# Kernel optimization log

Hardware: AMD Instinct MI355X
Metric: run time of the kernel (lower is better)

## Reference

```python
import jax, jax.numpy as jnp
import numpy as np

ROPE_BASE = 10000.0
NUM_HEADS = 16
NUM_KV_HEADS = 4


def _rms_norm(x, eps):
    # F.rms_norm with no weight: x / sqrt(mean(x^2) + eps)
    return x * jax.lax.rsqrt(jnp.mean(x * x, axis=-1, keepdims=True) + eps)


def _apply_rope(x, cos, sin):
    h = x.shape[-1] // 2
    x1, x2 = x[..., :h], x[..., h:]
    return jnp.concatenate([x1 * cos + x2 * sin, -x1 * sin + x2 * cos], axis=-1)


def setup_inputs() -> dict:
    key = jax.random.key(0)
    ks = jax.random.split(key, 5)
    B, T, D = 2, 2048, 1024
    H, Hkv = NUM_HEADS, NUM_KV_HEADS
    hd = D // H
    kv_dim = Hkv * hd
    s_in = 1.0 / np.sqrt(D)
    return {
        "x": jax.random.normal(ks[0], (B, T, D), dtype=jnp.float32),
        "Wq": jax.random.normal(ks[1], (D, D), dtype=jnp.float32) * s_in,
        "Wk": jax.random.normal(ks[2], (kv_dim, D), dtype=jnp.float32) * s_in,
        "Wv": jax.random.normal(ks[3], (kv_dim, D), dtype=jnp.float32) * s_in,
        "Wproj": jax.random.normal(ks[4], (D, D), dtype=jnp.float32) * s_in,
        "q_gain": jnp.full((H,), 1.0, dtype=jnp.float32),
    }


def reference(x, Wq, Wk, Wv, Wproj, q_gain):
    B, T, D = x.shape
    H, Hkv = NUM_HEADS, NUM_KV_HEADS
    hd = D // H
    rep = H // Hkv
    eps = jnp.finfo(x.dtype).eps

    # QKV projections (F.linear: x @ W.T)
    q = jnp.einsum('btd,od->bto', x, Wq).reshape(B, T, H, hd).transpose(0, 2, 1, 3)
    k = jnp.einsum('btd,od->bto', x, Wk).reshape(B, T, Hkv, hd).transpose(0, 2, 1, 3)
    v = jnp.einsum('btd,od->bto', x, Wv).reshape(B, T, Hkv, hd).transpose(0, 2, 1, 3)

    q = _rms_norm(q, eps)
    k = _rms_norm(k, eps)

    # RoPE tables: [1, 1, T, hd/2]
    inv_freq = 1.0 / (ROPE_BASE ** (jnp.arange(0, hd, 2, dtype=jnp.float32) / hd))
    f = jnp.arange(T, dtype=jnp.float32)[:, None] * inv_freq[None, :]
    cos = jnp.cos(f)[None, None].astype(q.dtype)
    sin = jnp.sin(f)[None, None].astype(q.dtype)
    q = _apply_rope(q, cos, sin)
    k = _apply_rope(k, cos, sin)

    q = q * q_gain.astype(q.dtype)[None, :, None, None]

    # GQA without materializing repeated K/V: group q heads [Hkv, rep]
    qg = q.reshape(B, Hkv, rep, T, hd)
    scale = hd ** -0.5
    scores = jnp.einsum('bgrqd,bgkd->bgrqk', qg, k) * scale
    causal = jnp.tril(jnp.ones((T, T), dtype=bool))
    scores = jnp.where(causal, scores, -jnp.inf)
    att = jax.nn.softmax(scores.astype(jnp.float32), axis=-1).astype(q.dtype)
    y = jnp.einsum('bgrqk,bgkd->bgrqd', att, v)  # [B,Hkv,rep,T,hd]
    y = y.reshape(B, H, T, hd).transpose(0, 2, 1, 3).reshape(B, T, D)
    return jnp.einsum('btd,od->bto', y, Wproj)
```

## Files before the change

kernel.cpp:

```cpp
#include <hip/hip_runtime.h>
#include <cstdint>
#include <cstddef>

typedef __attribute__((ext_vector_type(8))) short short8;
typedef __attribute__((ext_vector_type(4))) float floatx4;
typedef __attribute__((ext_vector_type(16))) float floatx16;
typedef __attribute__((ext_vector_type(4))) short short4v;
typedef unsigned short u16;
typedef unsigned int u32;

#define B_   2
#define T_   2048
#define D_   1024
#define H_   16
#define HKV_ 4
#define HD_  64
#define KV_  256
#define M_   4096
#define QS_  1536

#define NX   4194304
#define NWQ  1048576
#define NWK  262144
#define NWV  262144
#define NWP  1048576
#define NCAST (NX + NWQ + NWK + NWV + NWP)
#define CAST_BLOCKS (NCAST / 1024)
#define TAB_BLOCKS  256

__device__ __forceinline__ float b2f(u16 u) {
    union { u32 i; float f; } v; v.i = ((u32)u) << 16; return v.f;
}
__device__ __forceinline__ u16 f2b(float f) {
    union { float f; u32 i; } v; v.f = f;
    u32 r = v.i + 0x7FFF + ((v.i >> 16) & 1);
    return (u16)(r >> 16);
}
__device__ __forceinline__ u32 pack_hi(float a, float b) {
    union { float f; u32 u; } ua, ub; ua.f = a; ub.f = b;
    return (ua.u >> 16) | (ub.u & 0xFFFF0000u);
}

__device__ __forceinline__ void async16(const u16* g, u16* l) {
    __builtin_amdgcn_global_load_lds(
        (const __attribute__((address_space(1))) u32*)g,
        (__attribute__((address_space(3))) u32*)l, 16, 0, 0);
}

__device__ __forceinline__ u32 cvtpk(float lo, float hi) {
    u32 r;
    asm("v_cvt_pk_bf16_f32 %0, %1, %2" : "=v"(r) : "v"(lo), "v"(hi));
    return r;
}
__device__ __forceinline__ void swap32(u32& a, u32& b) {
    asm volatile("v_permlane32_swap_b32 %0, %1" : "+v"(a), "+v"(b));
}
__device__ __forceinline__ void swap32f(float& a, float& b) {
    asm volatile("v_permlane32_swap_b32 %0, %1" : "+v"(a), "+v"(b));
}
__device__ __forceinline__ short8 pkfrag(u32 w0, u32 w1, u32 w2, u32 w3) {
    union { u32 w[4]; short8 s; } u;
    u.w[0] = w0; u.w[1] = w1; u.w[2] = w2; u.w[3] = w3;
    return u.s;
}

__global__ __launch_bounds__(256) void prep(const float* __restrict__ x,
                                            const float* __restrict__ wq,
                                            const float* __restrict__ wk,
                                            const float* __restrict__ wv,
                                            const float* __restrict__ wp,
                                            u16* __restrict__ dst,
                                            float2* __restrict__ tab) {
    int blk = blockIdx.x;
    if (blk < CAST_BLOCKS) {
        int i = blk * 1024 + threadIdx.x * 4;
        const float* src; int off;
        if      (i < NX)                  { src = x;  off = i; }
        else if (i < NX+NWQ)              { src = wq; off = i - NX; }
        else if (i < NX+NWQ+NWK)          { src = wk; off = i - (NX+NWQ); }
        else if (i < NX+NWQ+NWK+NWV)      { src = wv; off = i - (NX+NWQ+NWK); }
        else                              { src = wp; off = i - (NX+NWQ+NWK+NWV); }
        float4 v = *(const float4*)(src + off);
        short4v o;
        o.x = (short)f2b(v.x); o.y = (short)f2b(v.y);
        o.z = (short)f2b(v.z); o.w = (short)f2b(v.w);
        *(short4v*)(dst + i) = o;
    } else {
        int idx = (blk - CAST_BLOCKS) * 256 + threadIdx.x;
        int t = idx >> 5, i = idx & 31;
        float freq = exp2f(-(float)i * (13.287712379549449f / 32.0f));
        float ang = (float)t * freq;
        tab[idx] = make_float2(cosf(ang), sinf(ang));
    }
}

__global__ __launch_bounds__(256, 3) void gemm_qkv(const u16* __restrict__ A,
                                                   const u16* __restrict__ W,
                                                   u16* __restrict__ C,
                                                   u16* __restrict__ Vt,
                                                   const float* __restrict__ gain,
                                                   const float2* __restrict__ tab) {
    const int K = D_;
    __shared__ u16 As[2][2][128 * 32];
    __shared__ u16 Bs[2][2][64 * 32];
    const int t = threadIdx.x;
    const int wave = t >> 6, lane = t & 63;
    const int quad = lane >> 4, l16 = lane & 15;
    const int wm = wave * 32;
    const int m0 = blockIdx.y * 128, n0 = blockIdx.x * 64;

    floatx4 acc[2][4];
#pragma unroll
    for (int i = 0; i < 2; i++)
#pragma unroll
        for (int j = 0; j < 4; j++) acc[i][j] = (floatx4){0.f, 0.f, 0.f, 0.f};

    const int sr = t >> 2, sc = (t & 3) * 8;
    const u16* ga = A + (size_t)(m0 + sr) * K + sc;
    const u16* gb = W + (size_t)(n0 + sr) * K + sc;

    auto stage = [&](int buf, int half, int koff) {
        async16(ga + koff, As[buf][half] + t * 8);
        async16(ga + koff + (size_t)64 * K, As[buf][half] + t * 8 + 64 * 32);
        async16(gb + koff, Bs[buf][half] + t * 8);
    };

    stage(0, 0, 0);
    stage(0, 1, 32);

    int cur = 0;
    for (int kt = 0; kt < K; kt += 64) {
        __syncthreads();
        if (kt + 64 < K) {
            stage(cur ^ 1, 0, kt + 64);
            stage(cur ^ 1, 1, kt + 96);
        }
#pragma unroll
        for (int half = 0; half < 2; half++) {
            short8 af[2], bf[4];
#pragma unroll
            for (int mt = 0; mt < 2; mt++)
                af[mt] = *(const short8*)(As[cur][half] + (wm + mt * 16 + l16) * 32 + quad * 8);
#pragma unroll
            for (int nt = 0; nt < 4; nt++)
                bf[nt] = *(const short8*)(Bs[cur][half] + (nt * 16 + l16) * 32 + quad * 8);
#pragma unroll
            for (int mt = 0; mt < 2; mt++)
#pragma unroll
                for (int nt = 0; nt < 4; nt++)
                    acc[mt][nt] = __builtin_amdgcn_mfma_f32_16x16x32_bf16(
                        af[mt], bf[nt], acc[mt][nt], 0, 0, 0);
        }
        cur ^= 1;
    }

    const int col0 = n0;
    if (col0 < 1280) {
        float gs = (col0 < 1024)
                 ? gain[col0 >> 6] * (0.125f * 1.4426950408889634f)
                 : 1.0f;
#pragma unroll
        for (int mt = 0; mt < 2; mt++)
#pragma unroll
            for (int r = 0; r < 4; r++) {
                int row = m0 + wm + mt * 16 + quad * 4 + r;
                int tt = row & (T_ - 1);
                float v0 = acc[mt][0][r], v1 = acc[mt][1][r];
                float v2 = acc[mt][2][r], v3 = acc[mt][3][r];
                float ss = v0 * v0 + v1 * v1 + v2 * v2 + v3 * v3;
                ss += __shfl_xor(ss, 1); ss += __shfl_xor(ss, 2);
                ss += __shfl_xor(ss, 4); ss += __shfl_xor(ss, 8);
                float inv = rsqrtf(ss * (1.0f / 64.0f) + 1.1920929e-7f);
                v0 *= inv; v1 *= inv; v2 *= inv; v3 *= inv;
                float2 cs0 = tab[tt * 32 + l16];
                float2 cs1 = tab[tt * 32 + 16 + l16];
                float o0 = (v0 * cs0.x + v2 * cs0.y) * gs;
                float o1 = (v1 * cs1.x + v3 * cs1.y) * gs;
                float o2 = (v2 * cs0.x - v0 * cs0.y) * gs;
                float o3 = (v3 * cs1.x - v1 * cs1.y) * gs;
                u16* cp = C + (size_t)row * QS_ + col0 + l16;
                cp[0]  = f2b(o0);
                cp[16] = f2b(o1);
                cp[32] = f2b(o2);
                cp[48] = f2b(o3);
            }
    } else {
        const int g = (col0 - 1280) >> 6;
#pragma unroll
        for (int mt = 0; mt < 2; mt++)
#pragma unroll
            for (int r = 0; r < 4; r++) {
                int row = m0 + wm + mt * 16 + quad * 4 + r;
                int tt = row & (T_ - 1);
                int bb = row >> 11;
#pragma unroll
                for (int nt = 0; nt < 4; nt++)
                    Vt[(size_t)((bb * 4 + g) * 64 + nt * 16 + l16) * T_ + tt] =
                        f2b(acc[mt][nt][r]);
            }
    }
}

__global__ __launch_bounds__(256, 3) void gemm_proj(const u16* __restrict__ A,
                                                    const u16* __restrict__ W,
                                                    float* __restrict__ C) {
    const int K = D_;
    __shared__ u16 As[2][2][128 * 32];
    __shared__ u16 Bs[2][2][64 * 32];
    const int t = threadIdx.x;
    const int wave = t >> 6, lane = t & 63;
    const int quad = lane >> 4, l16 = lane & 15;
    const int wm = wave * 32;
    const int m0 = blockIdx.y * 128, n0 = blockIdx.x * 64;

    floatx4 acc[2][4];
#pragma unroll
    for (int i = 0; i < 2; i++)
#pragma unroll
        for (int j = 0; j < 4; j++) acc[i][j] = (floatx4){0.f, 0.f, 0.f, 0.f};

    const int sr = t >> 2, sc = (t & 3) * 8;
    const u16* ga = A + (size_t)(m0 + sr) * K + sc;
    const u16* gb = W + (size_t)(n0 + sr) * K + sc;

    auto stage = [&](int buf, int half, int koff) {
        async16(ga + koff, As[buf][half] + t * 8);
        async16(ga + koff + (size_t)64 * K, As[buf][half] + t * 8 + 64 * 32);
        async16(gb + koff, Bs[buf][half] + t * 8);
    };

    stage(0, 0, 0);
    stage(0, 1, 32);

    int cur = 0;
    for (int kt = 0; kt < K; kt += 64) {
        __syncthreads();
        if (kt + 64 < K) {
            stage(cur ^ 1, 0, kt + 64);
            stage(cur ^ 1, 1, kt + 96);
        }
#pragma unroll
        for (int half = 0; half < 2; half++) {
            short8 af[2], bf[4];
#pragma unroll
            for (int mt = 0; mt < 2; mt++)
                af[mt] = *(const short8*)(As[cur][half] + (wm + mt * 16 + l16) * 32 + quad * 8);
#pragma unroll
            for (int nt = 0; nt < 4; nt++)
                bf[nt] = *(const short8*)(Bs[cur][half] + (nt * 16 + l16) * 32 + quad * 8);
#pragma unroll
            for (int mt = 0; mt < 2; mt++)
#pragma unroll
                for (int nt = 0; nt < 4; nt++)
                    acc[mt][nt] = __builtin_amdgcn_mfma_f32_16x16x32_bf16(
                        af[mt], bf[nt], acc[mt][nt], 0, 0, 0);
        }
        cur ^= 1;
    }

#pragma unroll
    for (int mt = 0; mt < 2; mt++)
#pragma unroll
        for (int nt = 0; nt < 4; nt++)
#pragma unroll
            for (int r = 0; r < 4; r++) {
                int row = m0 + wm + mt * 16 + quad * 4 + r;
                int col = n0 + nt * 16 + l16;
                C[(size_t)row * D_ + col] = acc[mt][nt][r];
            }
}

__global__ __launch_bounds__(256, 2) void flash(const u16* __restrict__ QKV,
                                                const u16* __restrict__ Vtr,
                                                float* __restrict__ Opart,
                                                float* __restrict__ Lpart) {
    const int u  = blockIdx.x;
    const int h  = blockIdx.y;
    const int b  = blockIdx.z;
    const int g  = h >> 2;
    const int w    = threadIdx.x >> 6;
    const int lane = threadIdx.x & 63;
    const int ln31 = lane & 31;
    const int hi   = lane >> 5;
    const int swz  = lane & 7;

    __shared__ u16 Kb[3][4096];
    __shared__ u16 Vb[3][4096];
    __shared__ float Ot[4][2048];

    const int srow = w * 16 + (lane >> 3);
    const int sseg = (lane & 7) ^ ((lane >> 3) & 7);
    const u16* kgb = QKV + (size_t)(b * T_ + srow) * QS_ + D_ + g * 64 + sseg * 8;
    const u16* vgb = Vtr + (size_t)((b * 4 + g) * 64 + srow) * T_ + sseg * 8;

    auto stage = [&](int tile, int bi) {
        const u16* kg = kgb + (size_t)tile * 64 * QS_;
        const u16* vg = vgb + (size_t)tile * 64;
        u16* kl = &Kb[bi][w * 1024 + lane * 8];
        u16* vl = &Vb[bi][w * 1024 + lane * 8];
        async16(kg, kl);
        async16(kg + (size_t)8 * QS_, kl + 512);
        async16(vg, vl);
        async16(vg + (size_t)8 * T_, vl + 512);
    };
    auto tileOf = [&](int gidx) { return (gidx <= u) ? gidx : gidx + 15 - 2 * u; };

    stage(tileOf(0), 0);
    stage(tileOf(1), 1);

    int gi = 0;
    for (int seg = 0; seg < 2; ++seg) {
        const int jt   = seg ? 15 - u : u;
        const int nIt  = seg ? 16 - u : u + 1;
        const int qrow = jt * 128 + w * 32 + ln31;

        const u16* qp = QKV + (size_t)(b * T_ + qrow) * QS_ + h * HD_;
        short8 aq[4];
#pragma unroll
        for (int kc = 0; kc < 4; kc++)
            aq[kc] = *(const short8*)(qp + kc * 16 + hi * 8);

        floatx16 acc[2];
#pragma unroll
        for (int dh = 0; dh < 2; dh++)
#pragma unroll
            for (int i = 0; i < 16; i++) acc[dh][i] = 0.f;
        float l = 0.f;

        for (int itn = 0; itn < nIt; ++itn, ++gi) {
            const int tk = tileOf(gi);
            if (gi == 16) asm volatile("s_waitcnt vmcnt(0)" ::: "memory");
            else          asm volatile("s_waitcnt vmcnt(4)" ::: "memory");
            __builtin_amdgcn_s_barrier();
            asm volatile("" ::: "memory");

            const int bc = gi % 3;
            if (gi + 2 <= 16) stage(tileOf(gi + 2), (gi + 2) % 3);

            const u16* Kp = &Kb[bc][0];
            const u16* Vp = &Vb[bc][0];
            short8 kf[2][4], vfr[2][4];
#pragma unroll
            for (int kh = 0; kh < 2; kh++)
#pragma unroll
                for (int kc = 0; kc < 4; kc++)
                    kf[kh][kc] = *(const short8*)(Kp + (kh * 32 + ln31) * 64 +
                                                  (((kc * 2 + hi) ^ swz) << 3));
#pragma unroll
            for (int dh = 0; dh < 2; dh++)
#pragma unroll
                for (int kc = 0; kc < 4; kc++)
                    vfr[dh][kc] = *(const short8*)(Vp + (dh * 32 + ln31) * 64 +
                                                   (((kc * 2 + hi) ^ swz) << 3));

            floatx16 s[2];
#pragma unroll
            for (int kh = 0; kh < 2; kh++)
#pragma unroll
                for (int i = 0; i < 16; i++) s[kh][i] = 0.f;

            __builtin_amdgcn_s_setprio(1);
#pragma unroll
            for (int kc = 0; kc < 4; kc++) {
                s[0] = __builtin_amdgcn_mfma_f32_32x32x16_bf16(kf[0][kc], aq[kc], s[0], 0, 0, 0);
                s[1] = __builtin_amdgcn_mfma_f32_32x32x16_bf16(kf[1][kc], aq[kc], s[1], 0, 0, 0);
            }
            __builtin_amdgcn_s_setprio(0);

            float p[2][16];
            if (tk >= 2 * jt) {
#pragma unroll
                for (int kh = 0; kh < 2; kh++)
#pragma unroll
                    for (int r = 0; r < 16; r++) {
                        int key = tk * 64 + kh * 32 + (r & 3) + ((r >> 2) << 3) + (hi << 2);
                        float e = __builtin_amdgcn_exp2f(s[kh][r]);
                        e = (key <= qrow) ? e : 0.f;
                        l += e; p[kh][r] = e;
                    }
            } else {
#pragma unroll
                for (int kh = 0; kh < 2; kh++)
#pragma unroll
                    for (int r = 0; r < 16; r++) {
                        float e = __builtin_amdgcn_exp2f(s[kh][r]);
                        l += e; p[kh][r] = e;
                    }
            }

            short8 pb[4];
#pragma unroll
            for (int kh = 0; kh < 2; kh++) {
                u32 a0 = cvtpk(p[kh][0], p[kh][1]),  b0 = cvtpk(p[kh][4], p[kh][5]);
                u32 c0 = cvtpk(p[kh][2], p[kh][3]),  d0 = cvtpk(p[kh][6], p[kh][7]);
                swap32(a0, b0); swap32(c0, d0);
                pb[kh * 2] = pkfrag(a0, c0, b0, d0);
                u32 a1 = cvtpk(p[kh][8],  p[kh][9]),  b1 = cvtpk(p[kh][12], p[kh][13]);
                u32 c1 = cvtpk(p[kh][10], p[kh][11]), d1 = cvtpk(p[kh][14], p[kh][15]);
                swap32(a1, b1); swap32(c1, d1);
                pb[kh * 2 + 1] = pkfrag(a1, c1, b1, d1);
            }

            __builtin_amdgcn_s_setprio(1);
#pragma unroll
            for (int kc = 0; kc < 4; kc++) {
                acc[0] = __builtin_amdgcn_mfma_f32_32x32x16_bf16(vfr[0][kc], pb[kc], acc[0], 0, 0, 0);
                acc[1] = __builtin_amdgcn_mfma_f32_32x32x16_bf16(vfr[1][kc], pb[kc], acc[1], 0, 0, 0);
            }
            __builtin_amdgcn_s_setprio(0);
        }

        float la = l, lb = l;
        swap32f(la, lb);
        float lt = la + lb;

        float* ot = &Ot[w][0];
#pragma unroll
        for (int dh = 0; dh < 2; dh++)
#pragma unroll
            for (int g4 = 0; g4 < 4; g4++) {
                int ss = (dh * 8 + g4 * 2 + hi) ^ (ln31 & 7);
                float4 v = make_float4(acc[dh][g4 * 4 + 0], acc[dh][g4 * 4 + 1],
                                       acc[dh][g4 * 4 + 2], acc[dh][g4 * 4 + 3]);
                *(float4*)(ot + ln31 * 64 + ss * 4) = v;
            }
        asm volatile("s_waitcnt lgkmcnt(0)" ::: "memory");

        const int hq = lane >> 4;
        const int s4 = lane & 15;
        float* obase = Opart + (size_t)seg * 4194304 +
                       ((size_t)(b * 2048 + jt * 128 + w * 32)) * 1024 + h * HD_;
#pragma unroll
        for (int it = 0; it < 8; it++) {
            int q2 = it * 4 + hq;
            int ss = s4 ^ (q2 & 7);
            float4 v = *(const float4*)(ot + q2 * 64 + ss * 4);
            *(float4*)(obase + (size_t)q2 * 1024 + s4 * 4) = v;
        }
        if (lane < 32)
            Lpart[((size_t)seg * 4096 + b * 2048 + jt * 128 + w * 32 + lane) * 16 + h] = lt;
    }
}

__global__ __launch_bounds__(256) void combine(const float* __restrict__ Opart,
                                               const float* __restrict__ Lpart,
                                               u16* __restrict__ Y) {
    int e = (blockIdx.x * 256 + threadIdx.x) * 4;
    int row = e >> 10, col = e & 1023;
    int li = row * 16 + (col >> 6);
    float l0 = Lpart[li];
    float l1 = Lpart[li + 4096 * 16];
    float inv = 1.0f / (l0 + l1);
    size_t oi = (size_t)row * 1024 + col;
    float4 o0 = *(const float4*)(Opart + oi);
    float4 o1 = *(const float4*)(Opart + oi + (size_t)4194304);
    short4v y;
    y.x = (short)f2b((o0.x + o1.x) * inv); y.y = (short)f2b((o0.y + o1.y) * inv);
    y.z = (short)f2b((o0.z + o1.z) * inv); y.w = (short)f2b((o0.w + o1.w) * inv);
    *(short4v*)(Y + (size_t)row * D_ + col) = y;
}

extern "C" void kernel_launch(void* const* d_in, const int* in_sizes, int n_in,
                              void* d_out, int out_size, void* d_ws, size_t ws_size,
                              hipStream_t stream) {
    const float* x    = (const float*)d_in[0];
    const float* Wq   = (const float*)d_in[1];
    const float* Wk   = (const float*)d_in[2];
    const float* Wv   = (const float*)d_in[3];
    const float* Wp   = (const float*)d_in[4];
    const float* gain = (const float*)d_in[5];
    float* out = (float*)d_out;

    u16* xb   = (u16*)d_ws;
    u16* Wcat = xb + (size_t)NX;
    u16* Wpb  = Wcat + (size_t)(NWQ + NWK + NWV);
    u16* QKV  = Wpb + (size_t)NWP;
    u16* Vt   = QKV + (size_t)M_ * QS_;
    u16* Y    = Vt + (size_t)M_ * KV_;
    float2* tab = (float2*)(Y + (size_t)M_ * D_);
    float* Opart = (float*)(tab + 65536);
    float* Lpart = Opart + (size_t)8 * 1024 * 1024;

    prep<<<CAST_BLOCKS + TAB_BLOCKS, 256, 0, stream>>>(x, Wq, Wk, Wv, Wp, xb, tab);

    gemm_qkv<<<dim3(QS_ / 64, M_ / 128), 256, 0, stream>>>(xb, Wcat, QKV, Vt,
                                                           gain, tab);

    flash<<<dim3(16, H_, B_), 256, 0, stream>>>(QKV, Vt, Opart, Lpart);

    combine<<<4096, 256, 0, stream>>>(Opart, Lpart, Y);

    gemm_proj<<<dim3(D_ / 64, M_ / 128), 256, 0, stream>>>(Y, Wpb, out);
}
```

Before: 164.5 us.

## Rebalance flash causal tiles, write low tiles directly, swizzle GEMM LDS layout

The causal work split in flash changes. Blocks with u<8 fully process query tile u and write the normalized bf16 output straight to Y. They then take the first part of tile 15-u, while blocks with u>=8 cover the rest of their own tile. Only the upper half of query rows now go through the Opart/Lpart partial buffers, which halves the combine kernel's work and the fp32 partial traffic. It also applies an XOR swizzle to the GEMM LDS tiles to cut bank conflicts on fragment reads, and packs softmax probabilities into bf16 pairs as they are computed. The tile-index mapping is intricate and risks load imbalance or indexing errors.

```diff
diff --git a/kernel.cpp b/kernel.cpp
--- a/kernel.cpp
+++ b/kernel.cpp
@@ -35,10 +35,6 @@
     union { float f; u32 i; } v; v.f = f;
     u32 r = v.i + 0x7FFF + ((v.i >> 16) & 1);
     return (u16)(r >> 16);
-}
-__device__ __forceinline__ u32 pack_hi(float a, float b) {
-    union { float f; u32 u; } ua, ub; ua.f = a; ub.f = b;
-    return (ua.u >> 16) | (ub.u & 0xFFFF0000u);
 }
 
 __device__ __forceinline__ void async16(const u16* g, u16* l) {
@@ -115,7 +111,8 @@
 #pragma unroll
         for (int j = 0; j < 4; j++) acc[i][j] = (floatx4){0.f, 0.f, 0.f, 0.f};
 
-    const int sr = t >> 2, sc = (t & 3) * 8;
+    const int sr = t >> 2;
+    const int sc = (((t & 3) ^ ((t >> 3) & 3)) * 8);
     const u16* ga = A + (size_t)(m0 + sr) * K + sc;
     const u16* gb = W + (size_t)(n0 + sr) * K + sc;
 
@@ -139,11 +136,17 @@
         for (int half = 0; half < 2; half++) {
             short8 af[2], bf[4];
 #pragma unroll
-            for (int mt = 0; mt < 2; mt++)
-                af[mt] = *(const short8*)(As[cur][half] + (wm + mt * 16 + l16) * 32 + quad * 8);
-#pragma unroll
-            for (int nt = 0; nt < 4; nt++)
-                bf[nt] = *(const short8*)(Bs[cur][half] + (nt * 16 + l16) * 32 + quad * 8);
+            for (int mt = 0; mt < 2; mt++) {
+                int row = wm + mt * 16 + l16;
+                af[mt] = *(const short8*)(As[cur][half] + row * 32 +
+                                          ((quad ^ ((row >> 1) & 3)) << 3));
+            }
+#pragma unroll
+            for (int nt = 0; nt < 4; nt++) {
+                int row = nt * 16 + l16;
+                bf[nt] = *(const short8*)(Bs[cur][half] + row * 32 +
+                                          ((quad ^ ((row >> 1) & 3)) << 3));
+            }
 #pragma unroll
             for (int mt = 0; mt < 2; mt++)
 #pragma unroll
@@ -219,7 +222,8 @@
 #pragma unroll
         for (int j = 0; j < 4; j++) acc[i][j] = (floatx4){0.f, 0.f, 0.f, 0.f};
 
-    const int sr = t >> 2, sc = (t & 3) * 8;
+    const int sr = t >> 2;
+    const int sc = (((t & 3) ^ ((t >> 3) & 3)) * 8);
     const u16* ga = A + (size_t)(m0 + sr) * K + sc;
     const u16* gb = W + (size_t)(n0 + sr) * K + sc;
 
@@ -243,11 +247,17 @@
         for (int half = 0; half < 2; half++) {
             short8 af[2], bf[4];
 #pragma unroll
-            for (int mt = 0; mt < 2; mt++)
-                af[mt] = *(const short8*)(As[cur][half] + (wm + mt * 16 + l16) * 32 + quad * 8);
-#pragma unroll
-            for (int nt = 0; nt < 4; nt++)
-                bf[nt] = *(const short8*)(Bs[cur][half] + (nt * 16 + l16) * 32 + quad * 8);
+            for (int mt = 0; mt < 2; mt++) {
+                int row = wm + mt * 16 + l16;
+                af[mt] = *(const short8*)(As[cur][half] + row * 32 +
+                                          ((quad ^ ((row >> 1) & 3)) << 3));
+            }
+#pragma unroll
+            for (int nt = 0; nt < 4; nt++) {
+                int row = nt * 16 + l16;
+                bf[nt] = *(const short8*)(Bs[cur][half] + row * 32 +
+                                          ((quad ^ ((row >> 1) & 3)) << 3));
+            }
 #pragma unroll
             for (int mt = 0; mt < 2; mt++)
 #pragma unroll
@@ -272,6 +282,7 @@
 
 __global__ __launch_bounds__(256, 2) void flash(const u16* __restrict__ QKV,
                                                 const u16* __restrict__ Vtr,
+                                                u16* __restrict__ Y,
                                                 float* __restrict__ Opart,
                                                 float* __restrict__ Lpart) {
     const int u  = blockIdx.x;
@@ -303,15 +314,21 @@
         async16(vg, vl);
         async16(vg + (size_t)8 * T_, vl + 512);
     };
-    auto tileOf = [&](int gidx) { return (gidx <= u) ? gidx : gidx + 15 - 2 * u; };
+    const bool low = (u < 8);
+    auto tileOf = [&](int gidx) {
+        return (low && gidx > 2 * u + 1) ? gidx + 15 - 2 * u : gidx;
+    };
 
     stage(tileOf(0), 0);
     stage(tileOf(1), 1);
 
+    const int nseg = low ? 2 : 1;
+    const int buf  = low ? 0 : 1;
     int gi = 0;
-    for (int seg = 0; seg < 2; ++seg) {
-        const int jt   = seg ? 15 - u : u;
-        const int nIt  = seg ? 16 - u : u + 1;
+    for (int seg = 0; seg < nseg; ++seg) {
+        const int jt   = (low && seg == 0) ? u : (low ? 15 - u : u);
+        const int nIt  = (low && seg == 0) ? 2 * u + 2 : (low ? 15 - 2 * u : 17);
+        const bool direct = low && (seg == 0);
         const int qrow = jt * 128 + w * 32 + ln31;
 
         const u16* qp = QKV + (size_t)(b * T_ + qrow) * QS_ + h * HD_;
@@ -367,36 +384,40 @@
             }
             __builtin_amdgcn_s_setprio(0);
 
-            float p[2][16];
+            u32 pw[2][8];
             if (tk >= 2 * jt) {
 #pragma unroll
                 for (int kh = 0; kh < 2; kh++)
 #pragma unroll
-                    for (int r = 0; r < 16; r++) {
-                        int key = tk * 64 + kh * 32 + (r & 3) + ((r >> 2) << 3) + (hi << 2);
-                        float e = __builtin_amdgcn_exp2f(s[kh][r]);
-                        e = (key <= qrow) ? e : 0.f;
-                        l += e; p[kh][r] = e;
+                    for (int i = 0; i < 8; i++) {
+                        int key0 = tk * 64 + kh * 32 +
+                                   ((2 * i) & 3) + (((2 * i) >> 2) << 3) + (hi << 2);
+                        float e0 = __builtin_amdgcn_exp2f(s[kh][2 * i]);
+                        float e1 = __builtin_amdgcn_exp2f(s[kh][2 * i + 1]);
+                        e0 = (key0 <= qrow) ? e0 : 0.f;
+                        e1 = (key0 + 1 <= qrow) ? e1 : 0.f;
+                        l += e0 + e1;
+                        pw[kh][i] = cvtpk(e0, e1);
                     }
             } else {
 #pragma unroll
                 for (int kh = 0; kh < 2; kh++)
 #pragma unroll
-                    for (int r = 0; r < 16; r++) {
-                        float e = __builtin_amdgcn_exp2f(s[kh][r]);
-                        l += e; p[kh][r] = e;
+                    for (int i = 0; i < 8; i++) {
+                        float e0 = __builtin_amdgcn_exp2f(s[kh][2 * i]);
+                        float e1 = __builtin_amdgcn_exp2f(s[kh][2 * i + 1]);
+                        l += e0 + e1;
+                        pw[kh][i] = cvtpk(e0, e1);
                     }
             }
 
             short8 pb[4];
 #pragma unroll
             for (int kh = 0; kh < 2; kh++) {
-                u32 a0 = cvtpk(p[kh][0], p[kh][1]),  b0 = cvtpk(p[kh][4], p[kh][5]);
-                u32 c0 = cvtpk(p[kh][2], p[kh][3]),  d0 = cvtpk(p[kh][6], p[kh][7]);
+                u32 a0 = pw[kh][0], b0 = pw[kh][2], c0 = pw[kh][1], d0 = pw[kh][3];
                 swap32(a0, b0); swap32(c0, d0);
                 pb[kh * 2] = pkfrag(a0, c0, b0, d0);
-                u32 a1 = cvtpk(p[kh][8],  p[kh][9]),  b1 = cvtpk(p[kh][12], p[kh][13]);
-                u32 c1 = cvtpk(p[kh][10], p[kh][11]), d1 = cvtpk(p[kh][14], p[kh][15]);
+                u32 a1 = pw[kh][4], b1 = pw[kh][6], c1 = pw[kh][5], d1 = pw[kh][7];
                 swap32(a1, b1); swap32(c1, d1);
                 pb[kh * 2 + 1] = pkfrag(a1, c1, b1, d1);
             }
@@ -413,6 +434,14 @@
         float la = l, lb = l;
         swap32f(la, lb);
         float lt = la + lb;
+
+        if (direct) {
+            float inv = 1.0f / lt;
+#pragma unroll
+            for (int dh = 0; dh < 2; dh++)
+#pragma unroll
+                for (int i = 0; i < 16; i++) acc[dh][i] *= inv;
+        }
 
         float* ot = &Ot[w][0];
 #pragma unroll
@@ -428,17 +457,32 @@
 
         const int hq = lane >> 4;
         const int s4 = lane & 15;
-        float* obase = Opart + (size_t)seg * 4194304 +
-                       ((size_t)(b * 2048 + jt * 128 + w * 32)) * 1024 + h * HD_;
-#pragma unroll
-        for (int it = 0; it < 8; it++) {
-            int q2 = it * 4 + hq;
-            int ss = s4 ^ (q2 & 7);
-            float4 v = *(const float4*)(ot + q2 * 64 + ss * 4);
-            *(float4*)(obase + (size_t)q2 * 1024 + s4 * 4) = v;
-        }
-        if (lane < 32)
-            Lpart[((size_t)seg * 4096 + b * 2048 + jt * 128 + w * 32 + lane) * 16 + h] = lt;
+        if (direct) {
+            u16* ybase = Y + (size_t)(b * T_ + jt * 128 + w * 32) * D_ + h * HD_;
+#pragma unroll
+            for (int it = 0; it < 8; it++) {
+                int q2 = it * 4 + hq;
+                int ss = s4 ^ (q2 & 7);
+                float4 v = *(const float4*)(ot + q2 * 64 + ss * 4);
+                uint2 yw;
+                yw.x = cvtpk(v.x, v.y);
+                yw.y = cvtpk(v.z, v.w);
+                *(uint2*)(ybase + (size_t)q2 * D_ + s4 * 4) = yw;
+            }
+        } else {
+            const int rp = jt * 128 + w * 32 - 1024;
+            float* obase = Opart + ((size_t)((buf * 2 + b) * 1024 + rp)) * 1024
+                         + h * HD_;
+#pragma unroll
+            for (int it = 0; it < 8; it++) {
+                int q2 = it * 4 + hq;
+                int ss = s4 ^ (q2 & 7);
+                float4 v = *(const float4*)(ot + q2 * 64 + ss * 4);
+                *(float4*)(obase + (size_t)q2 * 1024 + s4 * 4) = v;
+            }
+            if (hi == 0)
+                Lpart[((size_t)((buf * 2 + b) * 1024 + rp + ln31)) * 16 + h] = lt;
+        }
     }
 }
 
@@ -446,18 +490,20 @@
                                                const float* __restrict__ Lpart,
                                                u16* __restrict__ Y) {
     int e = (blockIdx.x * 256 + threadIdx.x) * 4;
-    int row = e >> 10, col = e & 1023;
-    int li = row * 16 + (col >> 6);
+    int b = e >> 20;
+    int rem = e & 1048575;
+    int row = rem >> 10, col = rem & 1023;
+    int li = (b * 1024 + row) * 16 + (col >> 6);
     float l0 = Lpart[li];
-    float l1 = Lpart[li + 4096 * 16];
+    float l1 = Lpart[li + 2 * 1024 * 16];
     float inv = 1.0f / (l0 + l1);
-    size_t oi = (size_t)row * 1024 + col;
+    size_t oi = ((size_t)(b * 1024 + row)) * 1024 + col;
     float4 o0 = *(const float4*)(Opart + oi);
-    float4 o1 = *(const float4*)(Opart + oi + (size_t)4194304);
+    float4 o1 = *(const float4*)(Opart + oi + (size_t)2 * 1024 * 1024);
     short4v y;
     y.x = (short)f2b((o0.x + o1.x) * inv); y.y = (short)f2b((o0.y + o1.y) * inv);
     y.z = (short)f2b((o0.z + o1.z) * inv); y.w = (short)f2b((o0.w + o1.w) * inv);
-    *(short4v*)(Y + (size_t)row * D_ + col) = y;
+    *(short4v*)(Y + (size_t)(b * T_ + 1024 + row) * D_ + col) = y;
 }
 
 extern "C" void kernel_launch(void* const* d_in, const int* in_sizes, int n_in,
@@ -479,16 +525,16 @@
     u16* Y    = Vt + (size_t)M_ * KV_;
     float2* tab = (float2*)(Y + (size_t)M_ * D_);
     float* Opart = (float*)(tab + 65536);
-    float* Lpart = Opart + (size_t)8 * 1024 * 1024;
+    float* Lpart = Opart + (size_t)4 * 1024 * 1024;
 
     prep<<<CAST_BLOCKS + TAB_BLOCKS, 256, 0, stream>>>(x, Wq, Wk, Wv, Wp, xb, tab);
 
     gemm_qkv<<<dim3(QS_ / 64, M_ / 128), 256, 0, stream>>>(xb, Wcat, QKV, Vt,
                                                            gain, tab);
 
-    flash<<<dim3(16, H_, B_), 256, 0, stream>>>(QKV, Vt, Opart, Lpart);
-
-    combine<<<4096, 256, 0, stream>>>(Opart, Lpart, Y);
+    flash<<<dim3(16, H_, B_), 256, 0, stream>>>(QKV, Vt, Y, Opart, Lpart);
+
+    combine<<<2048, 256, 0, stream>>>(Opart, Lpart, Y);
 
     gemm_proj<<<dim3(D_ / 64, M_ / 128), 256, 0, stream>>>(Y, Wpb, out);
 }
```

New measurement: 160.4 us. 2.5% less time.
